# Kernel tuning notes

Measured on AMD Instinct MI355X. Metric: run time of the kernel, lower is better.

## Reference

```python
import jax, jax.numpy as jnp
import numpy as np

N_QUBITS = 12
N_LAYERS = 6
BATCH = 8192
D_IN = 512


def _apply_1q(state, gate, wire):
    # state: [B] + [2]*n (real), gate: [2,2]. new[j] = sum_i gate[j,i]*old[i]
    s = jnp.moveaxis(state, 1 + wire, -1)
    s = jnp.einsum('...i,ji->...j', s, gate)
    return jnp.moveaxis(s, -1, 1 + wire)


def _apply_cnot(state, ctrl, tgt):
    # flip target amplitude pair where control bit == 1
    s = jnp.moveaxis(state, (1 + ctrl, 1 + tgt), (-2, -1))
    s = jnp.concatenate([s[..., :1, :], s[..., 1:, ::-1]], axis=-2)
    return jnp.moveaxis(s, (-2, -1), (1 + ctrl, 1 + tgt))


def _simulate(angles, weights):
    # angles: [B, n] per-sample RY angles; weights: [L, n] shared RY angles.
    # Circuit: H + RY(angle) per wire on |0>, then L x (RY layer + CNOT chain).
    # All gates are real -> real float32 statevector.
    B, n = angles.shape
    L = weights.shape[0]
    inv_sqrt2 = jnp.float32(1.0 / np.sqrt(2.0))
    half = 0.5 * angles
    c, s = jnp.cos(half), jnp.sin(half)
    # per-wire single-qubit state RY(a) @ H @ |0> = inv_sqrt2 * [c-s, c+s]
    v = inv_sqrt2 * jnp.stack([c - s, c + s], axis=-1)  # [B, n, 2]
    state = v[:, 0]  # [B, 2]
    for w in range(1, n):
        state = jnp.einsum('b...,bj->b...j', state, v[:, w])  # product state
    # state: [B] + [2]*n
    for layer in range(L):
        h = 0.5 * weights[layer]
        cl, sl = jnp.cos(h), jnp.sin(h)
        for w in range(n):
            gate = jnp.stack([jnp.stack([cl[w], -sl[w]]),
                              jnp.stack([sl[w], cl[w]])])
            state = _apply_1q(state, gate, w)
        for w in range(n - 1):
            state = _apply_cnot(state, w, w + 1)
    probs = state * state
    zs = []
    for w in range(n):
        axes = tuple(a for a in range(1, n + 1) if a != 1 + w)
        p = probs.sum(axis=axes)  # [B, 2]
        zs.append(p[:, 0] - p[:, 1])
    return jnp.stack(zs, axis=-1)  # [B, n] = <Z_i>


def setup_inputs() -> dict:
    key = jax.random.key(0)
    ks = jax.random.split(key, 6)
    x = jax.random.normal(ks[0], (BATCH, D_IN), jnp.float32)
    pre_w = jax.random.normal(ks[1], (N_QUBITS, D_IN), jnp.float32) / np.sqrt(D_IN)
    pre_b = jax.random.normal(ks[2], (N_QUBITS,), jnp.float32) * 0.01
    weights = jax.random.normal(ks[3], (N_LAYERS, N_QUBITS), jnp.float32)
    post_w = jax.random.normal(ks[4], (1, N_QUBITS), jnp.float32) / np.sqrt(N_QUBITS)
    post_b = jax.random.normal(ks[5], (1,), jnp.float32) * 0.01
    return {"x": x, "pre_w": pre_w, "pre_b": pre_b, "weights": weights,
            "post_w": post_w, "post_b": post_b}


def reference(x, pre_w, pre_b, weights, post_w, post_b):
    pre = x @ pre_w.T + pre_b                # [B, n_qubits]
    angles = pre * jnp.float32(np.pi / 2.0)  # RY(inputs[i]*pi/2)
    q_out = _simulate(angles, weights)       # [B, n_qubits]
    return q_out @ post_w.T + post_b         # [B, 1]
```

## Files before the change

kernel.cpp:

```cpp
#include <hip/hip_runtime.h>
#include <math.h>

#define NQ 12
#define NL 6
#define BATCHN 8192
#define DIN 512

typedef _Float16 f16;
typedef __attribute__((ext_vector_type(8)))  _Float16 f16x8;
typedef __attribute__((ext_vector_type(16))) float    f32x16;
typedef unsigned int u32;
typedef __attribute__((ext_vector_type(4))) u32 u32x4;
typedef __attribute__((ext_vector_type(2))) int i32x2;


__device__ __forceinline__ u32 pkrtz(float a, float b) {
  auto p = __builtin_amdgcn_cvt_pkrtz(a, b);
  return __builtin_bit_cast(u32, p);
}
__device__ __forceinline__ u32 bperm(int addr, u32 v) {
  return (u32)__builtin_amdgcn_ds_bpermute(addr, (int)v);
}
__device__ __forceinline__ float dppx1(float v) {
  return __int_as_float(__builtin_amdgcn_mov_dpp(__float_as_int(v), 0xB1, 0xF, 0xF, true));
}
__device__ __forceinline__ u32 dppx1u(u32 v) {
  return (u32)__builtin_amdgcn_mov_dpp((int)v, 0xB1, 0xF, 0xF, true);
}
__device__ __forceinline__ float dppx2(float v) {
  return __int_as_float(__builtin_amdgcn_mov_dpp(__float_as_int(v), 0x4E, 0xF, 0xF, true));
}
__device__ __forceinline__ float dppx8(float v) {
  return __int_as_float(__builtin_amdgcn_mov_dpp(__float_as_int(v), 0x128, 0xF, 0xF, true));
}
template <int PAT>
__device__ __forceinline__ float swzf(float v) {
  return __int_as_float(__builtin_amdgcn_ds_swizzle(__float_as_int(v), PAT));
}
__device__ __forceinline__ float wave_sum(float v) {
  v += dppx1(v);
  v += dppx2(v);
  v += swzf<0x101F>(v);
  v += dppx8(v);
  v += swzf<0x401F>(v);
  v += __shfl_xor(v, 32, 64);
  return v;
}
__device__ __forceinline__ f16x8 asf(const u32 a[4]) {
  u32x4 v; v.x = a[0]; v.y = a[1]; v.z = a[2]; v.w = a[3];
  return __builtin_bit_cast(f16x8, v);
}
__device__ __forceinline__ f16x8 ldB(const u32* __restrict__ p, int off) {
  u32x4 v = *(const u32x4*)(p + off);
  return __builtin_bit_cast(f16x8, v);
}

#if __has_builtin(__builtin_amdgcn_permlane32_swap)
__device__ __forceinline__ void pswap(u32& a, u32& b) {
  i32x2 r = __builtin_amdgcn_permlane32_swap((int)a, (int)b, false, false);
  a = (u32)r.x; b = (u32)r.y;
}
#else
#define PSWAP_FALLBACK 1
__device__ __forceinline__ void pswap_fb(u32& a, u32& b, bool hi, int axor) {
  u32 xa = bperm(axor, a), xb = bperm(axor, b);
  u32 na = hi ? xb : a;
  u32 nb = hi ? b : xa;
  a = na; b = nb;
}
#endif

__device__ __forceinline__ u32 foldw(u32 w, u32 m) {
  u32 partner = dppx1u(w);
  return (m & partner) | (~m & w);
}

__global__ void setup_mats(const float* __restrict__ weights, u32* __restrict__ Bbuf) {
  const int mm = blockIdx.x >> 3;
  const int l  = mm >> 1;
  const int qs = mm & 1;
  __shared__ float c6[6], s6[6];
  if (threadIdx.x < 6) {
    float h = 0.5f * weights[l * NQ + qs * 6 + threadIdx.x];
    c6[threadIdx.x] = cosf(h);
    s6[threadIdx.x] = sinf(h);
  }
  __syncthreads();
  const int t = (blockIdx.x & 7) * 256 + threadIdx.x;
  const int lane = (t >> 2) & 63;
  const int fk   = t >> 8;
  const int kt   = fk & 3;
  const int nt   = fk >> 2;
  const int n     = nt * 32 + (lane & 31);
  const int kbase = kt * 16 + (lane >> 5) * 8 + (t & 3) * 2;
  float v[2];
  #pragma unroll
  for (int u = 0; u < 2; ++u) {
    int k = kbase + u;
    int bb = k;
    if (l >= 1) { bb ^= bb << 1; bb ^= bb << 2; bb ^= bb << 4; bb &= 63; }
    float prod = 1.f;
    #pragma unroll
    for (int w = 0; w < 6; ++w) {
      const int aw = (n >> w) & 1, bw = (bb >> w) & 1;
      prod *= (aw == bw) ? c6[w] : (aw ? s6[w] : -s6[w]);
    }
    v[u] = prod;
  }
  Bbuf[mm * 2048 + t] = pkrtz(v[0], v[1]);
}

template <bool FOLD>
__device__ __forceinline__ void mm_step(f32x16 (&d)[2][2], const u32* __restrict__ Bl,
                                        bool hi, int axor, u32 maskA, u32 maskB) {
  u32 fr[2][4][4];
  #pragma unroll
  for (int kt = 0; kt < 4; ++kt) {
    const int s  = kt >> 1;
    const int b0 = 4 * ((2 * kt) & 3);
    const int b1 = 4 * ((2 * kt + 1) & 3);
    #pragma unroll
    for (int mt = 0; mt < 2; ++mt) {
      u32 p0a = pkrtz(d[s][mt][b0 + 0], d[s][mt][b0 + 1]);
      u32 p0b = pkrtz(d[s][mt][b0 + 2], d[s][mt][b0 + 3]);
      u32 p1a = pkrtz(d[s][mt][b1 + 0], d[s][mt][b1 + 1]);
      u32 p1b = pkrtz(d[s][mt][b1 + 2], d[s][mt][b1 + 3]);
      if (FOLD) {
        const int PAR4[4] = {0, 1, 1, 0};
        const int ka = (PAR4[b0 >> 2] + s) & 1;
        const int kc = (PAR4[b1 >> 2] + s) & 1;
        p0a = foldw(p0a, ka ? maskB : maskA);
        p0b = foldw(p0b, ka ? maskA : maskB);
        p1a = foldw(p1a, kc ? maskB : maskA);
        p1b = foldw(p1b, kc ? maskA : maskB);
      }
#ifdef PSWAP_FALLBACK
      pswap_fb(p0a, p1a, hi, axor);
      pswap_fb(p0b, p1b, hi, axor);
#else
      pswap(p0a, p1a);
      pswap(p0b, p1b);
#endif
      fr[mt][kt][0] = p0a;
      fr[mt][kt][1] = p0b;
      fr[mt][kt][2] = p1a;
      fr[mt][kt][3] = p1b;
    }
  }
  #pragma unroll
  for (int kt = 0; kt < 4; ++kt) {
    f16x8 A0 = asf(fr[0][kt]);
    f16x8 A1 = asf(fr[1][kt]);
    f16x8 B0 = ldB(Bl, (0 * 4 + kt) * 256);
    f16x8 B1 = ldB(Bl, (1 * 4 + kt) * 256);
    if (kt == 0) {
      f32x16 z{};
      d[0][0] = __builtin_amdgcn_mfma_f32_32x32x16_f16(A0, B0, z, 0, 0, 0);
      d[0][1] = __builtin_amdgcn_mfma_f32_32x32x16_f16(A0, B1, z, 0, 0, 0);
      d[1][0] = __builtin_amdgcn_mfma_f32_32x32x16_f16(A1, B0, z, 0, 0, 0);
      d[1][1] = __builtin_amdgcn_mfma_f32_32x32x16_f16(A1, B1, z, 0, 0, 0);
    } else {
      d[0][0] = __builtin_amdgcn_mfma_f32_32x32x16_f16(A0, B0, d[0][0], 0, 0, 0);
      d[0][1] = __builtin_amdgcn_mfma_f32_32x32x16_f16(A0, B1, d[0][1], 0, 0, 0);
      d[1][0] = __builtin_amdgcn_mfma_f32_32x32x16_f16(A1, B0, d[1][0], 0, 0, 0);
      d[1][1] = __builtin_amdgcn_mfma_f32_32x32x16_f16(A1, B1, d[1][1], 0, 0, 0);
    }
  }
}

__global__ void __launch_bounds__(256) __attribute__((amdgpu_waves_per_eu(4)))
dqc_main(const float* __restrict__ x,
         const float* __restrict__ pre_w,
         const float* __restrict__ pre_b,
         const float* __restrict__ post_w,
         const float* __restrict__ post_b,
         const u32* __restrict__ Bbuf,
         float* __restrict__ out)
{
  const int lane = threadIdx.x & 63;
  const bool hi  = lane >= 32;
  const int b    = blockIdx.x * 4 + (threadIdx.x >> 6);
  const int axor = (lane ^ 32) << 2;
  const u32 maskA = hi ? 0x0000FFFFu : 0xFFFF0000u;
  const u32 maskB = ~maskA;

  float acc[NQ];
  const float* xr = x + (size_t)b * DIN + lane * 8;
  const float4 xa = *(const float4*)(xr);
  const float4 xb = *(const float4*)(xr + 4);
  #pragma unroll
  for (int w = 0; w < NQ; ++w) {
    const float* wr = pre_w + w * DIN + lane * 8;
    const float4 wa = *(const float4*)(wr);
    const float4 wb = *(const float4*)(wr + 4);
    acc[w] = xa.x * wa.x + xa.y * wa.y + xa.z * wa.z + xa.w * wa.w
           + xb.x * wb.x + xb.y * wb.y + xb.z * wb.z + xb.w * wb.w;
  }
  #pragma unroll
  for (int w = 0; w < NQ; ++w) acc[w] = wave_sum(acc[w]);

  const float PI_4 = 0.78539816339744830962f;
  const float INV_SQRT2 = 0.70710678118654752440f;
  float v0[NQ], v1[NQ];
  #pragma unroll
  for (int w = 0; w < NQ; ++w) {
    float h = (acc[w] + pre_b[w]) * PI_4;
    float s, c;
    sincosf(h, &s, &c);
    v0[w] = (c - s) * INV_SQRT2;
    v1[w] = (c + s) * INV_SQRT2;
  }

  float base8[8];
  #pragma unroll
  for (int j = 0; j < 8; ++j)
    base8[j] = ((j & 1) ? v1[0] : v0[0]) * ((j & 2) ? v1[1] : v0[1]) * ((j & 4) ? v1[2] : v0[2]);
  float hiP[4];
  #pragma unroll
  for (int kt = 0; kt < 4; ++kt)
    hiP[kt] = (hi ? v1[3] : v0[3]) * ((kt & 1) ? v1[4] : v0[4]) * ((kt & 2) ? v1[5] : v0[5]);
  const float qb = ((lane & 1) ? v1[6] : v0[6]) * ((lane & 2) ? v1[7] : v0[7])
                 * ((lane & 4) ? v1[8] : v0[8]) * ((lane & 8) ? v1[9] : v0[9])
                 * ((lane & 16) ? v1[10] : v0[10]);
  const float qm0 = qb * v0[11], qm1 = qb * v1[11];

  f32x16 d[2][2];
  {
    const u32* Bl = Bbuf + lane * 4;
    #pragma unroll
    for (int kt = 0; kt < 4; ++kt) {
      u32 a0[4], a1[4];
      #pragma unroll
      for (int dw = 0; dw < 4; ++dw) {
        const float e0 = base8[2 * dw] * hiP[kt];
        const float e1 = base8[2 * dw + 1] * hiP[kt];
        a0[dw] = pkrtz(qm0 * e0, qm0 * e1);
        a1[dw] = pkrtz(qm1 * e0, qm1 * e1);
      }
      f16x8 A0 = asf(a0), A1 = asf(a1);
      f16x8 B0 = ldB(Bl, (0 * 4 + kt) * 256);
      f16x8 B1 = ldB(Bl, (1 * 4 + kt) * 256);
      if (kt == 0) {
        f32x16 z{};
        d[0][0] = __builtin_amdgcn_mfma_f32_32x32x16_f16(A0, B0, z, 0, 0, 0);
        d[0][1] = __builtin_amdgcn_mfma_f32_32x32x16_f16(A0, B1, z, 0, 0, 0);
        d[1][0] = __builtin_amdgcn_mfma_f32_32x32x16_f16(A1, B0, z, 0, 0, 0);
        d[1][1] = __builtin_amdgcn_mfma_f32_32x32x16_f16(A1, B1, z, 0, 0, 0);
      } else {
        d[0][0] = __builtin_amdgcn_mfma_f32_32x32x16_f16(A0, B0, d[0][0], 0, 0, 0);
        d[0][1] = __builtin_amdgcn_mfma_f32_32x32x16_f16(A0, B1, d[0][1], 0, 0, 0);
        d[1][0] = __builtin_amdgcn_mfma_f32_32x32x16_f16(A1, B0, d[1][0], 0, 0, 0);
        d[1][1] = __builtin_amdgcn_mfma_f32_32x32x16_f16(A1, B1, d[1][1], 0, 0, 0);
      }
    }
  }

  #pragma clang loop unroll(disable)
  for (int i = 0; i < 5; ++i) {
    mm_step<false>(d, Bbuf + (2 * i + 1) * 2048 + lane * 4, hi, axor, maskA, maskB);
    mm_step<true >(d, Bbuf + (2 * i + 2) * 2048 + lane * 4, hi, axor, maskA, maskB);
  }
  mm_step<false>(d, Bbuf + 11 * 2048 + lane * 4, hi, axor, maskA, maskB);

  float A0 = 0.f, A1 = 0.f, s00 = 0.f, s01 = 0.f;
  float zp0 = 0.f, zp1 = 0.f, zp3 = 0.f, zp4 = 0.f, zp5 = 0.f;
  #pragma unroll
  for (int mt = 0; mt < 2; ++mt)
    #pragma unroll
    for (int nt = 0; nt < 2; ++nt)
      #pragma unroll
      for (int r = 0; r < 16; ++r) {
        float v = d[mt][nt][r];
        float sq = v * v;
        const int par0 = (__builtin_popcount(r & 3) + __builtin_popcount(r >> 2) + mt) & 1;
        if (par0) A1 += sq; else A0 += sq;
        if (nt == 0) { if (par0) s01 += sq; else s00 += sq; }
        const int c0 = r & 1;
        const int c1 = (r ^ (r >> 1)) & 1;
        const int c3 = c1 ^ ((r >> 2) & 1);
        const int c4 = c3 ^ ((r >> 3) & 1);
        const int c5 = c4 ^ mt;
        zp0 += c0 ? -sq : sq;
        zp1 += c1 ? -sq : sq;
        zp3 += c3 ? -sq : sq;
        zp4 += c4 ? -sq : sq;
        zp5 += c5 ? -sq : sq;
      }
  const float sgnhi = hi ? -1.f : 1.f;
  const float tot   = A0 + A1;
  const float diff  = sgnhi * (A0 - A1);
  const float diffs = sgnhi * (2.f * (s00 - s01) - (A0 - A1));
  float z[12];
  z[0] = zp0;
  z[1] = zp1;
  z[2] = sgnhi * zp1;
  z[3] = sgnhi * zp3;
  z[4] = sgnhi * zp4;
  z[5] = sgnhi * zp5;
  #pragma unroll
  for (int j = 0; j < 5; ++j) {
    const int par = __builtin_popcount(lane & ((2 << j) - 1)) & 1;
    z[6 + j] = par ? -diff : diff;
  }
  {
    const int par = __builtin_popcount(lane & 31) & 1;
    z[11] = par ? -diffs : diffs;
  }
  const float tots = wave_sum(tot);
  #pragma unroll
  for (int w = 0; w < 12; ++w) z[w] = wave_sum(z[w]);

  if (lane == 0) {
    const float inv = 1.0f / tots;
    float o = post_b[0];
    #pragma unroll
    for (int w = 0; w < 12; ++w) o = fmaf(z[w] * inv, post_w[w], o);
    out[b] = o;
  }
}

extern "C" void kernel_launch(void* const* d_in, const int* in_sizes, int n_in,
                              void* d_out, int out_size, void* d_ws, size_t ws_size,
                              hipStream_t stream) {
  (void)in_sizes; (void)n_in; (void)out_size; (void)ws_size;
  const float* x       = (const float*)d_in[0];
  const float* pre_w   = (const float*)d_in[1];
  const float* pre_b   = (const float*)d_in[2];
  const float* weights = (const float*)d_in[3];
  const float* post_w  = (const float*)d_in[4];
  const float* post_b  = (const float*)d_in[5];
  float* out = (float*)d_out;
  u32* Bbuf = (u32*)d_ws;

  setup_mats<<<96, 256, 0, stream>>>(weights, Bbuf);
  dqc_main<<<BATCHN / 4, 256, 0, stream>>>(x, pre_w, pre_b, post_w, post_b, Bbuf, out);
}
```

Before: 129.4 us.

## Fold first RY layer and CNOT permutation into per-wire product-state construction

Applies the first layer's RY rotations directly to each wire's single-qubit amplitudes, since the initial state is a product state. The first CNOT chain's permutation is folded into how the A fragments are assembled, with lane and k-tile parity selecting the amplitudes. This lets the MFMA pipeline start from a later matrix stage and skip two mm_step stages per wave. In exchange there are extra per-thread sincos calls and selection logic, and the index remapping has to match the B-matrix layout exactly.

Result: no change. 131.0 us (+1.2%).

```diff
diff --git a/kernel.cpp b/kernel.cpp
--- a/kernel.cpp
+++ b/kernel.cpp
@@ -172,6 +172,7 @@
 dqc_main(const float* __restrict__ x,
          const float* __restrict__ pre_w,
          const float* __restrict__ pre_b,
+         const float* __restrict__ weights,
          const float* __restrict__ post_w,
          const float* __restrict__ post_b,
          const u32* __restrict__ Bbuf,
@@ -211,22 +212,37 @@
     v1[w] = (c + s) * INV_SQRT2;
   }
 
+  float u0[NQ], u1[NQ];
+  #pragma unroll
+  for (int w = 0; w < NQ; ++w) {
+    float s, c;
+    sincosf(0.5f * weights[w], &s, &c);
+    u0[w] = c * v0[w] - s * v1[w];
+    u1[w] = s * v0[w] + c * v1[w];
+  }
+
   float base8[8];
   #pragma unroll
   for (int j = 0; j < 8; ++j)
-    base8[j] = ((j & 1) ? v1[0] : v0[0]) * ((j & 2) ? v1[1] : v0[1]) * ((j & 4) ? v1[2] : v0[2]);
+    base8[j] = ((j & 1) ? u1[0] : u0[0]) * ((j & 2) ? u1[1] : u0[1]) * ((j & 4) ? u1[2] : u0[2]);
   float hiP[4];
   #pragma unroll
   for (int kt = 0; kt < 4; ++kt)
-    hiP[kt] = (hi ? v1[3] : v0[3]) * ((kt & 1) ? v1[4] : v0[4]) * ((kt & 2) ? v1[5] : v0[5]);
-  const float qb = ((lane & 1) ? v1[6] : v0[6]) * ((lane & 2) ? v1[7] : v0[7])
-                 * ((lane & 4) ? v1[8] : v0[8]) * ((lane & 8) ? v1[9] : v0[9])
-                 * ((lane & 16) ? v1[10] : v0[10]);
-  const float qm0 = qb * v0[11], qm1 = qb * v1[11];
+    hiP[kt] = (hi ? u1[3] : u0[3]) * ((kt & 1) ? u1[4] : u0[4]) * ((kt & 2) ? u1[5] : u0[5]);
+  const float q5 = ((lane & 2) ? u1[7] : u0[7]) * ((lane & 4) ? u1[8] : u0[8])
+                 * ((lane & 8) ? u1[9] : u0[9]) * ((lane & 16) ? u1[10] : u0[10]);
+  const float qA = q5 * ((lane & 1) ? u1[6] : u0[6]);
+  const float qB = q5 * ((lane & 1) ? u0[6] : u1[6]);
+  const float qeven = hi ? qB : qA;
+  const float qodd  = hi ? qA : qB;
+  const float qe0 = qeven * u0[11], qo0 = qodd * u0[11];
+  const float qe1 = qeven * u1[11], qo1 = qodd * u1[11];
 
   f32x16 d[2][2];
   {
-    const u32* Bl = Bbuf + lane * 4;
+    const u32* Bl = Bbuf + 2 * 2048 + lane * 4;
+    const int PKT[4] = {0, 1, 1, 0};
+    const int PDW[4] = {0, 1, 1, 0};
     #pragma unroll
     for (int kt = 0; kt < 4; ++kt) {
       u32 a0[4], a1[4];
@@ -234,8 +250,9 @@
       for (int dw = 0; dw < 4; ++dw) {
         const float e0 = base8[2 * dw] * hiP[kt];
         const float e1 = base8[2 * dw + 1] * hiP[kt];
-        a0[dw] = pkrtz(qm0 * e0, qm0 * e1);
-        a1[dw] = pkrtz(qm1 * e0, qm1 * e1);
+        const bool cls = (PKT[kt] ^ PDW[dw]) != 0;
+        a0[dw] = pkrtz((cls ? qo0 : qe0) * e0, (cls ? qe0 : qo0) * e1);
+        a1[dw] = pkrtz((cls ? qo1 : qe1) * e0, (cls ? qe1 : qo1) * e1);
       }
       f16x8 A0 = asf(a0), A1 = asf(a1);
       f16x8 B0 = ldB(Bl, (0 * 4 + kt) * 256);
@@ -256,9 +273,9 @@
   }
 
   #pragma clang loop unroll(disable)
-  for (int i = 0; i < 5; ++i) {
-    mm_step<false>(d, Bbuf + (2 * i + 1) * 2048 + lane * 4, hi, axor, maskA, maskB);
-    mm_step<true >(d, Bbuf + (2 * i + 2) * 2048 + lane * 4, hi, axor, maskA, maskB);
+  for (int i = 0; i < 4; ++i) {
+    mm_step<false>(d, Bbuf + (2 * i + 3) * 2048 + lane * 4, hi, axor, maskA, maskB);
+    mm_step<true >(d, Bbuf + (2 * i + 4) * 2048 + lane * 4, hi, axor, maskA, maskB);
   }
   mm_step<false>(d, Bbuf + 11 * 2048 + lane * 4, hi, axor, maskA, maskB);
 
@@ -333,5 +350,6 @@
   u32* Bbuf = (u32*)d_ws;
 
   setup_mats<<<96, 256, 0, stream>>>(weights, Bbuf);
-  dqc_main<<<BATCHN / 4, 256, 0, stream>>>(x, pre_w, pre_b, post_w, post_b, Bbuf, out);
-}
+  dqc_main<<<BATCHN / 4, 256, 0, stream>>>(x, pre_w, pre_b, weights,
+                                           post_w, post_b, Bbuf, out);
+}
```
